# Performance work log

Measured on AMD Instinct MI355X. Metric: run time of the kernel, lower is better.

Reference implementation:

```python
import jax, jax.numpy as jnp
import numpy as np

N = 50000      # num_nodes
R = 8          # num_relations
FIN = 128      # in_channels
H = 128        # hidden_channels
E = 800000     # num_edges (avg degree 16)


def _xavier(key, shape):
    fan_in, fan_out = shape[-2], shape[-1]
    lim = np.sqrt(6.0 / (fan_in + fan_out)).astype(np.float32)
    return jax.random.uniform(key, shape, jnp.float32, -lim, lim)


def setup_inputs() -> dict:
    key = jax.random.key(0)
    ks = jax.random.split(key, 10)
    return {
        "x": jax.random.normal(ks[0], (N, FIN), jnp.float32),
        "edge_index": jax.random.randint(ks[1], (2, E), 0, N, jnp.int32),
        "edge_type": jax.random.randint(ks[2], (E,), 0, R, jnp.int32),
        "rel_w0": _xavier(ks[3], (R, FIN, H)),
        "root_w0": _xavier(ks[4], (FIN, H)),
        "bias0": jnp.zeros((H,), jnp.float32),
        "rel_w1": _xavier(ks[5], (R, H, H)),
        "root_w1": _xavier(ks[6], (H, H)),
        "bias1": jnp.zeros((H,), jnp.float32),
        "rel_emb": _xavier(ks[7], (R, H)),
    }


def _rgcn_conv(x, src, dst, etype, rel_w, root_w, bias):
    # RGCNConv (PyG, aggr='mean'): out_i = root(x_i) + sum_r W_r * mean_{j in N_r(i)} x_j
    n = x.shape[0]
    seg = dst * R + etype                                   # fused (node, relation) segment id
    msgs = x[src]                                           # [E, F] gather
    sums = jax.ops.segment_sum(msgs, seg, num_segments=n * R)
    cnt = jax.ops.segment_sum(jnp.ones((src.shape[0], 1), x.dtype), seg, num_segments=n * R)
    mean = (sums / jnp.maximum(cnt, 1.0)).reshape(n, R, -1)  # [N, R, F]
    return jnp.einsum('nrf,rfh->nh', mean, rel_w) + x @ root_w + bias


def reference(x, edge_index, edge_type, rel_w0, root_w0, bias0,
              rel_w1, root_w1, bias1, rel_emb):
    src, dst = edge_index[0], edge_index[1]
    h = _rgcn_conv(x, src, dst, edge_type, rel_w0, root_w0, bias0)
    h = jax.nn.relu(h)  # dropout in eval mode (identity)
    h = _rgcn_conv(h, src, dst, edge_type, rel_w1, root_w1, bias1)
    return (h, rel_emb)
```

## Files before the change

kernel.cpp:

```cpp
#include <hip/hip_runtime.h>

typedef unsigned short ushort_t;
typedef __attribute__((ext_vector_type(8))) short short8;
typedef __attribute__((ext_vector_type(4))) float f32x4;
typedef __attribute__((ext_vector_type(4))) int int4v;

#define RNUM 8
#define FDIM 128

__device__ __forceinline__ float bf2f(ushort_t u) {
    union { unsigned int i; float f; } x;
    x.i = ((unsigned int)u) << 16;
    return x.f;
}
__device__ __forceinline__ ushort_t f2bf(float f) {
    union { float f; unsigned int i; } x;
    x.f = f;
    unsigned int u = x.i;
    u += 0x7fffu + ((u >> 16) & 1u);
    return (ushort_t)(u >> 16);
}


__global__ void init_head(int* __restrict__ head, int n) {
    int i = blockIdx.x * 256 + threadIdx.x;
    if (i < n) head[i] = -1;
}

__global__ void link_kernel(const int* __restrict__ src, const int* __restrict__ dst,
                            const int* __restrict__ et,
                            int* head, int2* __restrict__ meta, int E) {
    int i = blockIdx.x * 256 + threadIdx.x;
    if (i < E) {
        int seg = dst[i] * RNUM + et[i];
        int prev = atomicExch(&head[seg * 4 + (i & 3)], i);
        meta[i] = make_int2(src[i], prev);
    }
}


__global__ __launch_bounds__(256) void transpose_w(const float* __restrict__ rel_w0,
                                                   const float* __restrict__ root_w0,
                                                   const float* __restrict__ rel_w1,
                                                   const float* __restrict__ root_w1,
                                                   ushort_t* __restrict__ Wt) {
    int b = blockIdx.x;
    int layer = (b >= 9) ? 1 : 0;
    int r = b - layer * 9;
    const float* rel  = layer ? rel_w1 : rel_w0;
    const float* root = layer ? root_w1 : root_w0;
    const float* src = (r < 8) ? (rel + r * 16384) : root;
    __shared__ ushort_t t[128 * 130];
    for (int idx = threadIdx.x; idx < 16384; idx += 256)
        t[(idx >> 7) * 130 + (idx & 127)] = f2bf(src[idx]);
    __syncthreads();
    ushort_t* d = Wt + (layer * 9 + r) * 16384;
    for (int idx = threadIdx.x; idx < 16384; idx += 256)
        d[idx] = t[(idx & 127) * 130 + (idx >> 7)];
}


__global__ void cast_x(const float* __restrict__ x, ushort_t* __restrict__ xc,
                       int total, int totalPad) {
    int i = (blockIdx.x * 256 + threadIdx.x) * 8;
    if (i >= totalPad) return;
    ushort_t o[8];
    if (i < total) {
        float4 v0 = *(const float4*)(x + i);
        float4 v1 = *(const float4*)(x + i + 4);
        o[0] = f2bf(v0.x); o[1] = f2bf(v0.y); o[2] = f2bf(v0.z); o[3] = f2bf(v0.w);
        o[4] = f2bf(v1.x); o[5] = f2bf(v1.y); o[6] = f2bf(v1.z); o[7] = f2bf(v1.w);
    } else {
#pragma unroll
        for (int k = 0; k < 8; ++k) o[k] = 0;
    }
    *(int4v*)(xc + i) = *(int4v*)o;
}


__global__ __launch_bounds__(256) void seg_mean(const int4v* __restrict__ head4,
                                                const int2* __restrict__ meta,
                                                const ushort_t* __restrict__ X,
                                                ushort_t* __restrict__ Mm,
                                                int NSEG) {
    int t = blockIdx.x * 256 + threadIdx.x;
    int seg = t >> 4;
    int l16 = t & 15;
    if (seg >= NSEG) return;
    const ushort_t* gbase = X + l16 * 8;

    float acc[8];
#pragma unroll
    for (int k = 0; k < 8; ++k) acc[k] = 0.f;

    int4v h4 = head4[seg];
    int j[4], s[4], n[4];
#pragma unroll
    for (int c = 0; c < 4; ++c) j[c] = h4[c];
#pragma unroll
    for (int c = 0; c < 4; ++c)
        if (j[c] >= 0) { int2 m = meta[j[c]]; s[c] = m.x; n[c] = m.y; }

    int cnt = 0;
    while ((j[0] & j[1] & j[2] & j[3]) >= 0) {
        int4v v[4];
#pragma unroll
        for (int c = 0; c < 4; ++c)
            if (j[c] >= 0) v[c] = *(const int4v*)(gbase + ((size_t)s[c] << 7));
        int2 m2[4];
#pragma unroll
        for (int c = 0; c < 4; ++c)
            if (j[c] >= 0 && n[c] >= 0) m2[c] = meta[n[c]];
#pragma unroll
        for (int c = 0; c < 4; ++c) {
            if (j[c] >= 0) {
                const ushort_t* p = (const ushort_t*)&v[c];
#pragma unroll
                for (int k = 0; k < 8; ++k) acc[k] += bf2f(p[k]);
                ++cnt;
                j[c] = n[c];
                s[c] = m2[c].x;
                n[c] = m2[c].y;
            }
        }
    }

    float sc = (cnt > 0) ? 1.0f / (float)cnt : 0.f;
    ushort_t ov[8];
#pragma unroll
    for (int k = 0; k < 8; ++k) ov[k] = f2bf(acc[k] * sc);
    *(int4v*)(Mm + ((size_t)seg << 7) + l16 * 8) = *(int4v*)ov;
}


template <bool FINAL>
__global__ __launch_bounds__(512, 4) void rgcn_gemm(
    const ushort_t* __restrict__ Mm,
    const ushort_t* __restrict__ Xc,
    const ushort_t* __restrict__ Wt,
    const float* __restrict__ bias, float* __restrict__ outF,
    ushort_t* __restrict__ Xout, int N) {
    __shared__ ushort_t As[128 * 128];
    __shared__ ushort_t Bs[128 * 128];
    int tid = threadIdx.x;
    int wv = tid >> 6, lane = tid & 63;
    int l16 = lane & 15, q = lane >> 4;
    int nodeBase = blockIdx.x * 128;

    f32x4 acc[8];
#pragma unroll
    for (int ct = 0; ct < 8; ++ct) acc[ct] = (f32x4){0.f, 0.f, 0.f, 0.f};

    int4v aReg[4], bReg[4];

    auto issueLoads = [&](int r) {
#pragma unroll
        for (int i = 0; i < 4; ++i) {
            int L = i * 512 + tid;
            int row = L >> 4;
            int c = (L & 15) ^ (row & 15);
            const ushort_t* ga = (r < 8)
                ? Mm + ((size_t)(nodeBase + row) << 10) + r * 128 + c * 8
                : Xc + ((size_t)(nodeBase + row) << 7) + c * 8;
            aReg[i] = *(const int4v*)ga;
            bReg[i] = *(const int4v*)(Wt + r * 16384 + row * 128 + c * 8);
        }
    };
    auto writeLds = [&]() {
#pragma unroll
        for (int i = 0; i < 4; ++i) {
            int L = i * 512 + tid;
            *(int4v*)((char*)As + (size_t)L * 16) = aReg[i];
            *(int4v*)((char*)Bs + (size_t)L * 16) = bReg[i];
        }
    };

    issueLoads(0);
    writeLds();
    __syncthreads();

    for (int r = 0; r < 9; ++r) {
        if (r < 8) issueLoads(r + 1);
#pragma unroll
        for (int s = 0; s < 4; ++s) {
            int pos = ((s * 4 + q) ^ l16) * 16;
            short8 a = *(const short8*)((const char*)As + (wv * 16 + l16) * 256 + pos);
#pragma unroll
            for (int ct = 0; ct < 8; ++ct) {
                short8 b = *(const short8*)((const char*)Bs + (ct * 16 + l16) * 256 + pos);
                acc[ct] = __builtin_amdgcn_mfma_f32_16x16x32_bf16(a, b, acc[ct], 0, 0, 0);
            }
        }
        __syncthreads();
        if (r < 8) {
            writeLds();
            __syncthreads();
        }
    }

#pragma unroll
    for (int ct = 0; ct < 8; ++ct) {
        int h = ct * 16 + l16;
        float bv = bias[h];
#pragma unroll
        for (int reg = 0; reg < 4; ++reg) {
            int node = nodeBase + wv * 16 + q * 4 + reg;
            float v = acc[ct][reg] + bv;
            if (FINAL) {
                if (node < N) outF[(size_t)node * FDIM + h] = v;
            } else {
                Xout[(size_t)node * FDIM + h] =
                    (node < N) ? f2bf(fmaxf(v, 0.f)) : (ushort_t)0;
            }
        }
    }
}

__global__ void copy_emb(const float* __restrict__ e, float* __restrict__ out, int n) {
    int i = blockIdx.x * 256 + threadIdx.x;
    if (i < n) out[i] = e[i];
}


extern "C" void kernel_launch(void* const* d_in, const int* in_sizes, int n_in,
                              void* d_out, int out_size, void* d_ws, size_t ws_size,
                              hipStream_t stream) {
    const float* x        = (const float*)d_in[0];
    const int* edge_index = (const int*)d_in[1];
    const int* edge_type  = (const int*)d_in[2];
    const float* rel_w0   = (const float*)d_in[3];
    const float* root_w0  = (const float*)d_in[4];
    const float* bias0    = (const float*)d_in[5];
    const float* rel_w1   = (const float*)d_in[6];
    const float* root_w1  = (const float*)d_in[7];
    const float* bias1    = (const float*)d_in[8];
    const float* rel_emb  = (const float*)d_in[9];

    int N = in_sizes[0] / FDIM;
    int E = in_sizes[1] / 2;
    int NSEG = N * RNUM;
    const int* src = edge_index;
    const int* dst = edge_index + E;

    int nb_gemm = (N + 127) / 128;
    int NPAD = nb_gemm * 128;

    char* w = (char*)d_ws;
    auto alloc = [&](size_t bytes) -> char* {
        char* p = w;
        w += (bytes + 255) & ~(size_t)255;
        return p;
    };
    int* head     = (int*)alloc((size_t)NSEG * 4 * 4);
    int2* meta    = (int2*)alloc((size_t)E * 8);
    ushort_t* Wt  = (ushort_t*)alloc((size_t)2 * 9 * 16384 * 2);
    ushort_t* xc  = (ushort_t*)alloc((size_t)NPAD * FDIM * 2);
    ushort_t* h1c = (ushort_t*)alloc((size_t)NPAD * FDIM * 2);
    ushort_t* Mm  = (ushort_t*)alloc((size_t)NPAD * RNUM * FDIM * 2);
    (void)ws_size; (void)n_in; (void)out_size;

    int nb_head = (NSEG * 4 + 255) / 256;
    int nb_E    = (E + 255) / 256;
    int nb_mean = (NSEG * 16) / 256;
    int nb_cast = (NPAD * FDIM) / (256 * 8);

    init_head<<<nb_head, 256, 0, stream>>>(head, NSEG * 4);
    link_kernel<<<nb_E, 256, 0, stream>>>(src, dst, edge_type, head, meta, E);
    transpose_w<<<18, 256, 0, stream>>>(rel_w0, root_w0, rel_w1, root_w1, Wt);
    cast_x<<<nb_cast, 256, 0, stream>>>(x, xc, N * FDIM, NPAD * FDIM);

    seg_mean<<<nb_mean, 256, 0, stream>>>((const int4v*)head, meta, xc, Mm, NSEG);
    rgcn_gemm<false><<<nb_gemm, 512, 0, stream>>>(Mm, xc, Wt, bias0, nullptr, h1c, N);
    seg_mean<<<nb_mean, 256, 0, stream>>>((const int4v*)head, meta, h1c, Mm, NSEG);
    rgcn_gemm<true><<<nb_gemm, 512, 0, stream>>>(Mm, h1c, Wt + 9 * 16384, bias1,
                                                 (float*)d_out, nullptr, N);
    copy_emb<<<4, 256, 0, stream>>>(rel_emb, (float*)d_out + (size_t)N * FDIM,
                                    in_sizes[9]);
}
```

Measured before the change: 315.2 us.

## Fuse prologue kernels into one launch and double-buffer A loads in GEMM

Merges weight transpose, embedding copy, head init and x cast into a single block-dispatched prologue kernel, removing three launches and their gaps. In the RGCN GEMM, A-tile global loads are now issued two relations ahead into alternating register buffers, while B loads stay one step ahead. This deepens the prefetch to hide more global-memory latency, at the cost of extra VGPRs under launch_bounds(512,4), which may cause spills or lower occupancy.

```diff
diff --git a/kernel.cpp b/kernel.cpp
--- a/kernel.cpp
+++ b/kernel.cpp
@@ -21,11 +21,6 @@
     return (ushort_t)(u >> 16);
 }
 
-
-__global__ void init_head(int* __restrict__ head, int n) {
-    int i = blockIdx.x * 256 + threadIdx.x;
-    if (i < n) head[i] = -1;
-}
 
 __global__ void link_kernel(const int* __restrict__ src, const int* __restrict__ dst,
                             const int* __restrict__ et,
@@ -39,42 +34,50 @@
 }
 
 
-__global__ __launch_bounds__(256) void transpose_w(const float* __restrict__ rel_w0,
-                                                   const float* __restrict__ root_w0,
-                                                   const float* __restrict__ rel_w1,
-                                                   const float* __restrict__ root_w1,
-                                                   ushort_t* __restrict__ Wt) {
-    int b = blockIdx.x;
-    int layer = (b >= 9) ? 1 : 0;
-    int r = b - layer * 9;
-    const float* rel  = layer ? rel_w1 : rel_w0;
-    const float* root = layer ? root_w1 : root_w0;
-    const float* src = (r < 8) ? (rel + r * 16384) : root;
+__global__ __launch_bounds__(256) void prologue_fused(
+    const float* __restrict__ rel_w0, const float* __restrict__ root_w0,
+    const float* __restrict__ rel_w1, const float* __restrict__ root_w1,
+    ushort_t* __restrict__ Wt,
+    const float* __restrict__ x, ushort_t* __restrict__ xc,
+    int total, int totalPad,
+    int* __restrict__ head, int nhead,
+    const float* __restrict__ emb, float* __restrict__ outEmb, int nemb,
+    int nbHead) {
     __shared__ ushort_t t[128 * 130];
-    for (int idx = threadIdx.x; idx < 16384; idx += 256)
-        t[(idx >> 7) * 130 + (idx & 127)] = f2bf(src[idx]);
-    __syncthreads();
-    ushort_t* d = Wt + (layer * 9 + r) * 16384;
-    for (int idx = threadIdx.x; idx < 16384; idx += 256)
-        d[idx] = t[(idx & 127) * 130 + (idx >> 7)];
-}
-
-
-__global__ void cast_x(const float* __restrict__ x, ushort_t* __restrict__ xc,
-                       int total, int totalPad) {
-    int i = (blockIdx.x * 256 + threadIdx.x) * 8;
-    if (i >= totalPad) return;
-    ushort_t o[8];
-    if (i < total) {
-        float4 v0 = *(const float4*)(x + i);
-        float4 v1 = *(const float4*)(x + i + 4);
-        o[0] = f2bf(v0.x); o[1] = f2bf(v0.y); o[2] = f2bf(v0.z); o[3] = f2bf(v0.w);
-        o[4] = f2bf(v1.x); o[5] = f2bf(v1.y); o[6] = f2bf(v1.z); o[7] = f2bf(v1.w);
+    int b = blockIdx.x, tid = threadIdx.x;
+    if (b < 18) {
+        int layer = (b >= 9) ? 1 : 0;
+        int r = b - layer * 9;
+        const float* rel  = layer ? rel_w1 : rel_w0;
+        const float* root = layer ? root_w1 : root_w0;
+        const float* src = (r < 8) ? (rel + r * 16384) : root;
+        for (int idx = tid; idx < 16384; idx += 256)
+            t[(idx >> 7) * 130 + (idx & 127)] = f2bf(src[idx]);
+        __syncthreads();
+        ushort_t* d = Wt + (layer * 9 + r) * 16384;
+        for (int idx = tid; idx < 16384; idx += 256)
+            d[idx] = t[(idx & 127) * 130 + (idx >> 7)];
+    } else if (b == 18) {
+        for (int i = tid; i < nemb; i += 256) outEmb[i] = emb[i];
+    } else if (b < 19 + nbHead) {
+        int i = (b - 19) * 256 + tid;
+        if (i < nhead) head[i] = -1;
     } else {
-#pragma unroll
-        for (int k = 0; k < 8; ++k) o[k] = 0;
-    }
-    *(int4v*)(xc + i) = *(int4v*)o;
+        int i = ((b - 19 - nbHead) * 256 + tid) * 8;
+        if (i < totalPad) {
+            ushort_t o[8];
+            if (i < total) {
+                float4 v0 = *(const float4*)(x + i);
+                float4 v1 = *(const float4*)(x + i + 4);
+                o[0] = f2bf(v0.x); o[1] = f2bf(v0.y); o[2] = f2bf(v0.z); o[3] = f2bf(v0.w);
+                o[4] = f2bf(v1.x); o[5] = f2bf(v1.y); o[6] = f2bf(v1.z); o[7] = f2bf(v1.w);
+            } else {
+#pragma unroll
+                for (int k = 0; k < 8; ++k) o[k] = 0;
+            }
+            *(int4v*)(xc + i) = *(int4v*)o;
+        }
+    }
 }
 
 
@@ -151,9 +154,9 @@
 #pragma unroll
     for (int ct = 0; ct < 8; ++ct) acc[ct] = (f32x4){0.f, 0.f, 0.f, 0.f};
 
-    int4v aReg[4], bReg[4];
-
-    auto issueLoads = [&](int r) {
+    int4v aR0[4], aR1[4], bR[4];
+
+    auto loadA = [&](int4v* dstReg, int r) {
 #pragma unroll
         for (int i = 0; i < 4; ++i) {
             int L = i * 512 + tid;
@@ -162,25 +165,36 @@
             const ushort_t* ga = (r < 8)
                 ? Mm + ((size_t)(nodeBase + row) << 10) + r * 128 + c * 8
                 : Xc + ((size_t)(nodeBase + row) << 7) + c * 8;
-            aReg[i] = *(const int4v*)ga;
-            bReg[i] = *(const int4v*)(Wt + r * 16384 + row * 128 + c * 8);
-        }
-    };
-    auto writeLds = [&]() {
+            dstReg[i] = *(const int4v*)ga;
+        }
+    };
+    auto loadB = [&](int r) {
+#pragma unroll
+        for (int i = 0; i < 4; ++i) {
+            int L = i * 512 + tid;
+            int row = L >> 4;
+            int c = (L & 15) ^ (row & 15);
+            bR[i] = *(const int4v*)(Wt + r * 16384 + row * 128 + c * 8);
+        }
+    };
+    auto writeLds = [&](int4v* aReg) {
 #pragma unroll
         for (int i = 0; i < 4; ++i) {
             int L = i * 512 + tid;
             *(int4v*)((char*)As + (size_t)L * 16) = aReg[i];
-            *(int4v*)((char*)Bs + (size_t)L * 16) = bReg[i];
-        }
-    };
-
-    issueLoads(0);
-    writeLds();
+            *(int4v*)((char*)Bs + (size_t)L * 16) = bR[i];
+        }
+    };
+
+    loadA(aR0, 0);
+    loadB(0);
+    loadA(aR1, 1);
+    writeLds(aR0);
     __syncthreads();
 
     for (int r = 0; r < 9; ++r) {
-        if (r < 8) issueLoads(r + 1);
+        if (r < 7) loadA((r & 1) ? aR1 : aR0, r + 2);
+        if (r < 8) loadB(r + 1);
 #pragma unroll
         for (int s = 0; s < 4; ++s) {
             int pos = ((s * 4 + q) ^ l16) * 16;
@@ -193,7 +207,7 @@
         }
         __syncthreads();
         if (r < 8) {
-            writeLds();
+            writeLds(((r + 1) & 1) ? aR1 : aR0);
             __syncthreads();
         }
     }
@@ -214,11 +228,6 @@
             }
         }
     }
-}
-
-__global__ void copy_emb(const float* __restrict__ e, float* __restrict__ out, int n) {
-    int i = blockIdx.x * 256 + threadIdx.x;
-    if (i < n) out[i] = e[i];
 }
 
 
@@ -259,21 +268,24 @@
     ushort_t* Mm  = (ushort_t*)alloc((size_t)NPAD * RNUM * FDIM * 2);
     (void)ws_size; (void)n_in; (void)out_size;
 
-    int nb_head = (NSEG * 4 + 255) / 256;
+    int nhead   = NSEG * 4;
+    int nb_head = (nhead + 255) / 256;
     int nb_E    = (E + 255) / 256;
     int nb_mean = (NSEG * 16) / 256;
     int nb_cast = (NPAD * FDIM) / (256 * 8);
-
-    init_head<<<nb_head, 256, 0, stream>>>(head, NSEG * 4);
+    int nb_pro  = 19 + nb_head + nb_cast;
+
+    prologue_fused<<<nb_pro, 256, 0, stream>>>(
+        rel_w0, root_w0, rel_w1, root_w1, Wt,
+        x, xc, N * FDIM, NPAD * FDIM,
+        head, nhead,
+        rel_emb, (float*)d_out + (size_t)N * FDIM, in_sizes[9],
+        nb_head);
     link_kernel<<<nb_E, 256, 0, stream>>>(src, dst, edge_type, head, meta, E);
-    transpose_w<<<18, 256, 0, stream>>>(rel_w0, root_w0, rel_w1, root_w1, Wt);
-    cast_x<<<nb_cast, 256, 0, stream>>>(x, xc, N * FDIM, NPAD * FDIM);
 
     seg_mean<<<nb_mean, 256, 0, stream>>>((const int4v*)head, meta, xc, Mm, NSEG);
     rgcn_gemm<false><<<nb_gemm, 512, 0, stream>>>(Mm, xc, Wt, bias0, nullptr, h1c, N);
     seg_mean<<<nb_mean, 256, 0, stream>>>((const int4v*)head, meta, h1c, Mm, NSEG);
     rgcn_gemm<true><<<nb_gemm, 512, 0, stream>>>(Mm, h1c, Wt + 9 * 16384, bias1,
                                                  (float*)d_out, nullptr, N);
-    copy_emb<<<4, 256, 0, stream>>>(rel_emb, (float*)d_out + (size_t)N * FDIM,
-                                    in_sizes[9]);
-}
+}
```

After: 341.9 us. +8.5%, slower.
